# Kernel tuning notes

Measured on AMD Instinct MI355X. Metric: run time of the kernel, lower is better.

Reference implementation:

```python
import jax, jax.numpy as jnp
import numpy as np

D_MODEL = 1024
N_HEADS = 16
D_FF = 4096
D_K = D_MODEL // N_HEADS


def _ln(x, g, b, eps=1e-5):
    mu = jnp.mean(x, axis=-1, keepdims=True)
    var = jnp.mean(jnp.square(x - mu), axis=-1, keepdims=True)
    return (x - mu) * jax.lax.rsqrt(var + eps) * g + b


def setup_inputs() -> dict:
    key = jax.random.key(0)
    ks = jax.random.split(key, 16)
    s = 0.02
    inp = {
        "x": jax.random.normal(ks[0], (2, 2048, D_MODEL), dtype=jnp.float32),
        "Wq": jax.random.normal(ks[1], (D_MODEL, D_MODEL), dtype=jnp.float32) * s,
        "bq": jnp.zeros((D_MODEL,), jnp.float32),
        "Wk": jax.random.normal(ks[2], (D_MODEL, D_MODEL), dtype=jnp.float32) * s,
        "bk": jnp.zeros((D_MODEL,), jnp.float32),
        "Wv": jax.random.normal(ks[3], (D_MODEL, D_MODEL), dtype=jnp.float32) * s,
        "bv": jnp.zeros((D_MODEL,), jnp.float32),
        "Wo": jax.random.normal(ks[4], (D_MODEL, D_MODEL), dtype=jnp.float32) * s,
        "bo": jnp.zeros((D_MODEL,), jnp.float32),
        "W1": jax.random.normal(ks[5], (D_MODEL, D_FF), dtype=jnp.float32) * s,
        "b1": jnp.zeros((D_FF,), jnp.float32),
        "W2": jax.random.normal(ks[6], (D_FF, D_MODEL), dtype=jnp.float32) * s,
        "b2": jnp.zeros((D_MODEL,), jnp.float32),
        "g1": jnp.ones((D_MODEL,), jnp.float32),
        "be1": jnp.zeros((D_MODEL,), jnp.float32),
        "g2": jnp.ones((D_MODEL,), jnp.float32),
        "be2": jnp.zeros((D_MODEL,), jnp.float32),
    }
    return inp


def reference(x, Wq, bq, Wk, bk, Wv, bv, Wo, bo, W1, b1, W2, b2, g1, be1, g2, be2):
    B, L, D = x.shape
    # QKV projections -> [B, H, L, d_k]
    q = (x @ Wq + bq).reshape(B, L, N_HEADS, D_K).transpose(0, 2, 1, 3)
    k = (x @ Wk + bk).reshape(B, L, N_HEADS, D_K).transpose(0, 2, 1, 3)
    v = (x @ Wv + bv).reshape(B, L, N_HEADS, D_K).transpose(0, 2, 1, 3)
    scores = jnp.einsum("bhqd,bhkd->bhqk", q, k) / jnp.sqrt(jnp.float32(D_K))
    attn = jax.nn.softmax(scores, axis=-1)
    ctx = jnp.einsum("bhqk,bhkd->bhqd", attn, v)
    ctx = ctx.transpose(0, 2, 1, 3).reshape(B, L, D)
    attn_out = ctx @ Wo + bo
    # residual + LN1
    h = _ln(x + attn_out, g1, be1)
    # FFN (exact GELU, matching torch F.gelu default)
    ff = jax.nn.gelu(h @ W1 + b1, approximate=False) @ W2 + b2
    return _ln(h + ff, g2, be2)
```

## Files before the change

kernel.cpp:

```cpp
#include <hip/hip_runtime.h>
#include <cmath>


typedef unsigned short u16;
typedef unsigned int u32;
typedef __attribute__((ext_vector_type(8))) __bf16 bf16x8;
typedef __attribute__((ext_vector_type(4))) float f32x4;

#define MFMA16(a, b, c) __builtin_amdgcn_mfma_f32_16x16x32_bf16(a, b, c, 0, 0, 0)

__device__ __forceinline__ u16 f2bf(float f) {
  u32 u = __builtin_bit_cast(u32, f);
  u += 0x7fffu + ((u >> 16) & 1u);
  return (u16)(u >> 16);
}

__device__ __forceinline__ u32 packtrunc(float lo, float hi) {
#if __has_builtin(__builtin_amdgcn_perm)
  return __builtin_amdgcn_perm(__builtin_bit_cast(u32, hi),
                               __builtin_bit_cast(u32, lo), 0x07060302u);
#else
  return (__builtin_bit_cast(u32, lo) >> 16) |
         (__builtin_bit_cast(u32, hi) & 0xFFFF0000u);
#endif
}

__device__ __forceinline__ bf16x8 ld_frag(const u16* p) {
  return __builtin_bit_cast(bf16x8, *(const uint4*)p);
}

__device__ __forceinline__ float fexp2(float x) {
#if __has_builtin(__builtin_amdgcn_exp2f)
  return __builtin_amdgcn_exp2f(x);
#else
  return exp2f(x);
#endif
}

__device__ __forceinline__ void gload16(const u16* g, u16* l) {
  __builtin_amdgcn_global_load_lds(
      (const __attribute__((address_space(1))) void*)g,
      (__attribute__((address_space(3))) void*)l, 16, 0, 0);
}

#define WAITVL(N) asm volatile("s_waitcnt vmcnt(" #N ") lgkmcnt(0)" ::: "memory")
#define BAR() do { __builtin_amdgcn_s_barrier(); asm volatile("" ::: "memory"); } while (0)

__global__ __launch_bounds__(256) void cvt_bf16_k(const float* __restrict__ src,
                                                  u16* __restrict__ dst) {
  int i = (blockIdx.x * 256 + threadIdx.x) * 4;
  float4 v = *(const float4*)(src + i);
  ushort4 o;
  o.x = f2bf(v.x); o.y = f2bf(v.y); o.z = f2bf(v.z); o.w = f2bf(v.w);
  *(ushort4*)(dst + i) = o;
}

__global__ __launch_bounds__(256) void transpose_bf16_k(const float* __restrict__ src,
                                                        u16* __restrict__ dst,
                                                        int R, int C) {
  __shared__ float tile[32][33];
  int tx = threadIdx.x & 31, ty = threadIdx.x >> 5;
  int c0 = blockIdx.x * 32, r0 = blockIdx.y * 32;
#pragma unroll
  for (int i = 0; i < 4; i++)
    tile[ty + 8 * i][tx] = src[(long)(r0 + ty + 8 * i) * C + c0 + tx];
  __syncthreads();
#pragma unroll
  for (int i = 0; i < 4; i++)
    dst[(long)(c0 + ty + 8 * i) * R + r0 + tx] = f2bf(tile[tx][ty + 8 * i]);
}

__global__ __launch_bounds__(256) void transpose4_bf16_k(
    const float* __restrict__ Wq, const float* __restrict__ Wk,
    const float* __restrict__ Wv, const float* __restrict__ Wo,
    u16* __restrict__ wqkvT, u16* __restrict__ woT) {
  const int z = blockIdx.z;
  const float* src = (z == 0) ? Wq : (z == 1) ? Wk : (z == 2) ? Wv : Wo;
  u16* dst = (z < 3) ? (wqkvT + (size_t)z * 1024 * 1024) : woT;
  __shared__ float tile[32][33];
  int tx = threadIdx.x & 31, ty = threadIdx.x >> 5;
  int c0 = blockIdx.x * 32, r0 = blockIdx.y * 32;
#pragma unroll
  for (int i = 0; i < 4; i++)
    tile[ty + 8 * i][tx] = src[(long)(r0 + ty + 8 * i) * 1024 + c0 + tx];
  __syncthreads();
#pragma unroll
  for (int i = 0; i < 4; i++)
    dst[(long)(c0 + ty + 8 * i) * 1024 + r0 + tx] = f2bf(tile[tx][ty + 8 * i]);
}

template <int MODE>
__global__ __launch_bounds__(512, 2) void gemm256_k(
    const u16* __restrict__ A, const u16* __restrict__ BT,
    int N, int lda, int ldb, int Kc,
    const float* __restrict__ bias, float* __restrict__ outF, u16* __restrict__ outB,
    float* __restrict__ p1, float* __restrict__ p2, float* __restrict__ p3,
    u16* __restrict__ qd, u16* __restrict__ kd, u16* __restrict__ vTd,
    const float* __restrict__ bq, const float* __restrict__ bk, const float* __restrict__ bv) {
  __shared__ u16 As[4][256 * 32];
  __shared__ u16 Bs[4][256 * 32];
  const int tid = threadIdx.x;
  const int wave = tid >> 6, lane = tid & 63, quad = lane >> 4, l16 = lane & 15;
  const int wm = wave >> 2, wn = wave & 3;
  const int m0 = blockIdx.y * 256, n0 = blockIdx.x * 256;
  const int kz = blockIdx.z;
  const long kofs = (long)kz * Kc;
  const int KT = Kc >> 5;

  const int srow = lane >> 2;
  const int sseg = (lane & 3) ^ (srow & 3);
  const u16* aS = A + (long)(m0 + wave * 32 + srow) * lda + kofs + sseg * 8;
  const u16* bS = BT + (long)(n0 + wave * 32 + srow) * ldb + kofs + sseg * 8;

  auto stageA = [&](int sb, int s) {
    const u16* p = aS + (long)s * 32;
    gload16(p, &As[sb][wave * 1024]);
    gload16(p + 16 * (long)lda, &As[sb][wave * 1024 + 512]);
  };
  auto stageB = [&](int sb, int s) {
    const u16* p = bS + (long)s * 32;
    gload16(p, &Bs[sb][wave * 1024]);
    gload16(p + 16 * (long)ldb, &Bs[sb][wave * 1024 + 512]);
  };

  int aro[8], bro[4];
#pragma unroll
  for (int mf = 0; mf < 8; mf++) {
    int r = wm * 128 + mf * 16 + l16;
    aro[mf] = r * 32 + ((quad ^ (r & 3)) * 8);
  }
#pragma unroll
  for (int nf = 0; nf < 4; nf++) {
    int r = wn * 64 + nf * 16 + l16;
    bro[nf] = r * 32 + ((quad ^ (r & 3)) * 8);
  }

  f32x4 acc[8][4] = {};

  stageA(0, 0); stageB(0, 0);
  stageA(1, 1); stageB(1, 1);
  stageA(2, 2); stageB(2, 2);

#pragma unroll 1
  for (int t = 0; t < KT; ++t) {
    const int buf = t & 3;
    if (t < KT - 2)      { WAITVL(8); }
    else if (t == KT - 2){ WAITVL(4); }
    else                 { WAITVL(0); }
    BAR();

    bf16x8 af[4], bf4[4];
#pragma unroll
    for (int i = 0; i < 4; i++) af[i] = ld_frag(&As[buf][aro[i]]);
#pragma unroll
    for (int i = 0; i < 4; i++) bf4[i] = ld_frag(&Bs[buf][bro[i]]);
    if (t + 3 < KT) stageA((t + 3) & 3, t + 3);
    BAR();
    __builtin_amdgcn_s_setprio(1);
#pragma unroll
    for (int mf = 0; mf < 4; mf++)
#pragma unroll
      for (int nf = 0; nf < 4; nf++)
        acc[mf][nf] = MFMA16(af[mf], bf4[nf], acc[mf][nf]);
    __builtin_amdgcn_s_setprio(0);

    bf16x8 ag[4];
#pragma unroll
    for (int i = 0; i < 4; i++) ag[i] = ld_frag(&As[buf][aro[4 + i]]);
    if (t + 3 < KT) stageB((t + 3) & 3, t + 3);
    BAR();
    __builtin_amdgcn_s_setprio(1);
#pragma unroll
    for (int mf = 0; mf < 4; mf++)
#pragma unroll
      for (int nf = 0; nf < 4; nf++)
        acc[4 + mf][nf] = MFMA16(ag[mf], bf4[nf], acc[4 + mf][nf]);
    __builtin_amdgcn_s_setprio(0);
  }

  if (MODE == 0) {
    const int nbase = n0 + wn * 64;
    const int mat = nbase >> 10;
    const float* bp = (mat == 0) ? bq : ((mat == 1) ? bk : bv);
    float bb[4];
    int hh0[4], dd0[4];
#pragma unroll
    for (int nf = 0; nf < 4; nf++) {
      int nn = (nbase + nf * 16 + l16) & 1023;
      bb[nf] = bp[nn];
      hh0[nf] = nn >> 6;
      dd0[nf] = nn & 63;
    }
    if (mat < 2) {
#pragma unroll
      for (int mf = 0; mf < 8; mf++) {
#pragma unroll
        for (int r = 0; r < 4; r++) {
          int mr = m0 + wm * 128 + mf * 16 + quad * 4 + r;
          int bI = mr >> 11, ll = mr & 2047;
#pragma unroll
          for (int nf = 0; nf < 4; nf++) {
            float v = acc[mf][nf][r] + bb[nf];
            long idx = ((long)((bI * 16 + hh0[nf]) * 2048 + ll)) * 64 + dd0[nf];
            if (mat == 0) {
              qd[idx] = f2bf(v * 0.18033688011112043f);
            } else {
              kd[idx] = f2bf(v);
            }
          }
        }
      }
    } else {
#pragma unroll
      for (int nf = 0; nf < 4; nf++) {
#pragma unroll
        for (int mf = 0; mf < 8; mf++) {
#pragma unroll
          for (int r = 0; r < 4; r++) {
            int mr = m0 + wm * 128 + mf * 16 + quad * 4 + r;
            int bI = mr >> 11, ll = mr & 2047;
            float v = acc[mf][nf][r] + bb[nf];
            vTd[((long)((bI * 16 + hh0[nf]) * 64 + dd0[nf])) * 2048 + ll] = f2bf(v);
          }
        }
      }
    }
  } else if (MODE == 2) {
    float bb[4];
#pragma unroll
    for (int nf = 0; nf < 4; nf++) bb[nf] = bias[n0 + wn * 64 + nf * 16 + l16];
#pragma unroll
    for (int mf = 0; mf < 8; mf++) {
#pragma unroll
      for (int r = 0; r < 4; r++) {
        int mr = m0 + wm * 128 + mf * 16 + quad * 4 + r;
        u16* orow = outB + (long)mr * N + n0 + wn * 64 + l16;
#pragma unroll
        for (int nf = 0; nf < 4; nf++) {
          float v = acc[mf][nf][r] + bb[nf];
          v = 0.5f * v * (1.0f + erff(v * 0.70710678118654752f));
          orow[nf * 16] = f2bf(v);
        }
      }
    }
  } else {
    float* sl = (kz == 0) ? outF : (kz == 1) ? p1 : (kz == 2) ? p2 : p3;
#pragma unroll
    for (int mf = 0; mf < 8; mf++) {
#pragma unroll
      for (int r = 0; r < 4; r++) {
        int mr = m0 + wm * 128 + mf * 16 + quad * 4 + r;
        float* orow = sl + (long)mr * N + n0 + wn * 64 + l16;
#pragma unroll
        for (int nf = 0; nf < 4; nf++) orow[nf * 16] = acc[mf][nf][r];
      }
    }
  }
}

template <int MODE, int TN>
__global__ __launch_bounds__(256) void gemm_k(
    const u16* __restrict__ A, const u16* __restrict__ BT, int M, int N, int K,
    const float* __restrict__ bias, float* __restrict__ outF, u16* __restrict__ outB,
    u16* __restrict__ qd, u16* __restrict__ kd, u16* __restrict__ vTd,
    const float* __restrict__ bq, const float* __restrict__ bk, const float* __restrict__ bv) {
  constexpr int NT = TN / 32;
  __shared__ u16 As[2][128 * 32];
  __shared__ u16 Bs[2][TN * 32];
  const int tid = threadIdx.x;
  const int wave = tid >> 6, lane = tid & 63, quad = lane >> 4, l16 = lane & 15;
  const int wm = wave >> 1, wn = wave & 1;
  const int m0 = blockIdx.y * 128, n0 = blockIdx.x * TN;

  const int srow = lane >> 2;
  const int sxor = (lane & 3) ^ (srow & 3);
  const u16* aS0 = A + (long)(m0 + wave * 32 + srow) * K + sxor * 8;
  const u16* aS1 = aS0 + 16 * K;
  const u16* bS0 = BT + (long)(n0 + (TN == 128 ? wave * 32 : wave * 16) + srow) * K + sxor * 8;
  const u16* bS1 = bS0 + 16 * K;

  int aoff[4], boff[NT];
#pragma unroll
  for (int t = 0; t < 4; t++) {
    int ra = wm * 64 + t * 16 + l16;
    aoff[t] = ra * 32 + ((quad ^ (l16 & 3)) * 8);
  }
#pragma unroll
  for (int t = 0; t < NT; t++) {
    int rb = wn * (TN / 2) + t * 16 + l16;
    boff[t] = rb * 32 + ((quad ^ (l16 & 3)) * 8);
  }

  auto stage = [&](int buf, int k0) {
    gload16(aS0 + k0, &As[buf][(wave * 2 + 0) * 512]);
    gload16(aS1 + k0, &As[buf][(wave * 2 + 1) * 512]);
    if (TN == 128) {
      gload16(bS0 + k0, &Bs[buf][(wave * 2 + 0) * 512]);
      gload16(bS1 + k0, &Bs[buf][(wave * 2 + 1) * 512]);
    } else {
      gload16(bS0 + k0, &Bs[buf][wave * 512]);
    }
  };

  f32x4 acc[4][NT] = {};

  stage(0, 0);
#pragma unroll 1
  for (int k0 = 0; k0 < K; k0 += 32) {
    const int buf = (k0 >> 5) & 1;
    __syncthreads();
    if (k0 + 32 < K) stage(buf ^ 1, k0 + 32);
    bf16x8 af[4], bfr[NT];
#pragma unroll
    for (int t = 0; t < 4; t++) af[t] = ld_frag(&As[buf][aoff[t]]);
#pragma unroll
    for (int t = 0; t < NT; t++) bfr[t] = ld_frag(&Bs[buf][boff[t]]);
#pragma unroll
    for (int mt = 0; mt < 4; mt++)
#pragma unroll
      for (int nt = 0; nt < NT; nt++)
        acc[mt][nt] = MFMA16(af[mt], bfr[nt], acc[mt][nt]);
  }

  if (MODE == 1) {
    float bb[NT];
#pragma unroll
    for (int nt = 0; nt < NT; nt++) bb[nt] = bias[n0 + wn * (TN / 2) + nt * 16 + l16];
#pragma unroll
    for (int mt = 0; mt < 4; mt++) {
#pragma unroll
      for (int r = 0; r < 4; r++) {
        int mr = m0 + wm * 64 + mt * 16 + quad * 4 + r;
        float* orow = outF + (long)mr * N + n0 + wn * (TN / 2) + l16;
#pragma unroll
        for (int nt = 0; nt < NT; nt++)
          orow[nt * 16] = acc[mt][nt][r] + bb[nt];
      }
    }
  }
}

__global__ __launch_bounds__(256) void attn_k(const u16* __restrict__ qd,
                                              const u16* __restrict__ kd,
                                              const u16* __restrict__ vTd,
                                              float* __restrict__ oP0,
                                              float* __restrict__ oP1,
                                              float* __restrict__ ml0,
                                              float* __restrict__ ml1) {
  __shared__ u16 Ks[2][64 * 64];
  __shared__ u16 Vs[2][64 * 64];
  __shared__ __align__(16) u16 P[4][32][72];
  const int tid = threadIdx.x;
  const int wave = tid >> 6, lane = tid & 63, quad = lane >> 4, l16 = lane & 15;
  const int bh = blockIdx.y;
  const int kz = blockIdx.z;
  const int jbeg = kz * 1024, jend = jbeg + 1024;
  const u16* Q = qd + (long)bh * 2048 * 64;
  const u16* Kp = kd + (long)bh * 2048 * 64;
  const u16* Vt = vTd + (long)bh * 64 * 2048;
  const int qbase = blockIdx.x * 128 + wave * 32;

  bf16x8 qf[2][2];
#pragma unroll
  for (int qs = 0; qs < 2; qs++) {
    qf[qs][0] = ld_frag(Q + (qbase + qs * 16 + l16) * 64 + quad * 8);
    qf[qs][1] = ld_frag(Q + (qbase + qs * 16 + l16) * 64 + 32 + quad * 8);
  }

  f32x4 o[2][4] = {};
  float m[2] = {-1e30f, -1e30f}, l[2] = {0.f, 0.f};

  const int srow = lane >> 3;
  const int sx = (lane & 7) ^ srow;
  const int kr0 = wave * 16 + srow;
  const int kr1 = wave * 16 + 8 + srow;

  const int fs0 = ((0 * 4 + quad) ^ (l16 & 7)) * 8;
  const int fs1 = ((1 * 4 + quad) ^ (l16 & 7)) * 8;

  auto stage = [&](int buf, int j0) {
    gload16(Kp + (long)(j0 + kr0) * 64 + sx * 8, &Ks[buf][(wave * 2 + 0) * 512]);
    gload16(Kp + (long)(j0 + kr1) * 64 + sx * 8, &Ks[buf][(wave * 2 + 1) * 512]);
    gload16(Vt + (long)kr0 * 2048 + j0 + sx * 8, &Vs[buf][(wave * 2 + 0) * 512]);
    gload16(Vt + (long)kr1 * 2048 + j0 + sx * 8, &Vs[buf][(wave * 2 + 1) * 512]);
  };

  stage(0, jbeg);

#pragma unroll 1
  for (int j0 = jbeg; j0 < jend; j0 += 64) {
    const int buf = (j0 >> 6) & 1;
    __syncthreads();
    if (j0 + 64 < jend) stage(buf ^ 1, j0 + 64);

    const u16* kb = &Ks[buf][0];
    f32x4 st[2][4];
#pragma unroll
    for (int f = 0; f < 4; f++) {
      bf16x8 k0 = ld_frag(kb + (f * 16 + l16) * 64 + fs0);
      bf16x8 k1 = ld_frag(kb + (f * 16 + l16) * 64 + fs1);
      f32x4 s0 = {}, s1 = {};
      s0 = MFMA16(k0, qf[0][0], s0); s0 = MFMA16(k1, qf[0][1], s0);
      s1 = MFMA16(k0, qf[1][0], s1); s1 = MFMA16(k1, qf[1][1], s1);
      st[0][f] = s0; st[1][f] = s1;
    }

#pragma unroll
    for (int qs = 0; qs < 2; qs++) {
      float mx = -1e30f;
#pragma unroll
      for (int f = 0; f < 4; f++)
        mx = fmaxf(mx, fmaxf(fmaxf(st[qs][f][0], st[qs][f][1]),
                             fmaxf(st[qs][f][2], st[qs][f][3])));
      mx = fmaxf(mx, __shfl_xor(mx, 16));
      mx = fmaxf(mx, __shfl_xor(mx, 32));
      if (__any(mx > m[qs] + 8.0f)) {
        float mn = fmaxf(m[qs], mx);
        float al = fexp2(m[qs] - mn);
        m[qs] = mn;
        l[qs] *= al;
#pragma unroll
        for (int nt = 0; nt < 4; nt++) {
          o[qs][nt][0] *= al; o[qs][nt][1] *= al;
          o[qs][nt][2] *= al; o[qs][nt][3] *= al;
        }
      }
      float sm = 0.f;
      u16* prow = &P[wave][qs * 16 + l16][0];
#pragma unroll
      for (int f = 0; f < 4; f++) {
        float p0 = fexp2(st[qs][f][0] - m[qs]);
        float p1 = fexp2(st[qs][f][1] - m[qs]);
        float p2 = fexp2(st[qs][f][2] - m[qs]);
        float p3 = fexp2(st[qs][f][3] - m[qs]);
        sm += (p0 + p1) + (p2 + p3);
        uint2 u;
        u.x = packtrunc(p0, p1);
        u.y = packtrunc(p2, p3);
        *(uint2*)(prow + f * 16 + quad * 4) = u;
      }
      sm += __shfl_xor(sm, 16);
      sm += __shfl_xor(sm, 32);
      l[qs] += sm;
    }
    __asm__ volatile("s_waitcnt lgkmcnt(0)" ::: "memory");

    const u16* vb = &Vs[buf][0];
    bf16x8 vf[4][2];
#pragma unroll
    for (int nt = 0; nt < 4; nt++) {
      vf[nt][0] = ld_frag(vb + (nt * 16 + l16) * 64 + fs0);
      vf[nt][1] = ld_frag(vb + (nt * 16 + l16) * 64 + fs1);
    }
#pragma unroll
    for (int qs = 0; qs < 2; qs++) {
      const u16* prow = &P[wave][qs * 16 + l16][0];
#pragma unroll
      for (int kh = 0; kh < 2; kh++) {
        bf16x8 pf = ld_frag(prow + kh * 32 + quad * 8);
#pragma unroll
        for (int nt = 0; nt < 4; nt++)
          o[qs][nt] = MFMA16(vf[nt][kh], pf, o[qs][nt]);
      }
    }
  }

  float* oDst = kz ? oP1 : oP0;
  float* mlDst = kz ? ml1 : ml0;
#pragma unroll
  for (int qs = 0; qs < 2; qs++) {
    const long row = (long)bh * 2048 + qbase + qs * 16 + l16;
#pragma unroll
    for (int nt = 0; nt < 4; nt++)
      *(float4*)(oDst + row * 64 + nt * 16 + quad * 4) =
          *(const float4*)&o[qs][nt];
    if (quad == 0) {
      float2 ml2 = {m[qs], l[qs]};
      *(float2*)(mlDst + row * 2) = ml2;
    }
  }
}

__global__ __launch_bounds__(256) void attn_combine_k(
    const float* __restrict__ o0, const float* __restrict__ o1,
    const float* __restrict__ ml0, const float* __restrict__ ml1,
    u16* __restrict__ ctx) {
  long i = ((long)blockIdx.x * 256 + threadIdx.x) * 4;
  long row = i >> 6;
  int d = (int)(i & 63);
  float2 a0 = *(const float2*)(ml0 + row * 2);
  float2 a1 = *(const float2*)(ml1 + row * 2);
  float M = fmaxf(a0.x, a1.x);
  float w0 = fexp2(a0.x - M), w1 = fexp2(a1.x - M);
  float rinv = 1.0f / (a0.y * w0 + a1.y * w1);
  float4 v0 = *(const float4*)(o0 + i);
  float4 v1 = *(const float4*)(o1 + i);
  int bh = (int)(row >> 11), ll = (int)(row & 2047);
  int bI = bh >> 4, hh = bh & 15;
  ushort4 w;
  w.x = f2bf((v0.x * w0 + v1.x * w1) * rinv);
  w.y = f2bf((v0.y * w0 + v1.y * w1) * rinv);
  w.z = f2bf((v0.z * w0 + v1.z * w1) * rinv);
  w.w = f2bf((v0.w * w0 + v1.w * w1) * rinv);
  *(ushort4*)(ctx + ((long)(bI * 2048 + ll) * 1024) + hh * 64 + d) = w;
}

__global__ __launch_bounds__(256) void ln_k(const float* __restrict__ a,
                                            const float* __restrict__ b,
                                            const float* __restrict__ g,
                                            const float* __restrict__ be,
                                            float* __restrict__ outF,
                                            u16* __restrict__ outB) {
  const int row = blockIdx.x, tid = threadIdx.x;
  const float* pa = a + (long)row * 1024;
  const float* pb = b + (long)row * 1024;
  float v[4], s = 0.f, sq = 0.f;
#pragma unroll
  for (int i = 0; i < 4; i++) {
    int c = i * 256 + tid;
    v[i] = pa[c] + pb[c];
    s += v[i];
    sq += v[i] * v[i];
  }
#pragma unroll
  for (int off = 1; off < 64; off <<= 1) {
    s += __shfl_xor(s, off);
    sq += __shfl_xor(sq, off);
  }
  __shared__ float red[10];
  int wave = tid >> 6, lane = tid & 63;
  if (lane == 0) { red[wave * 2] = s; red[wave * 2 + 1] = sq; }
  __syncthreads();
  if (tid == 0) {
    float S = red[0] + red[2] + red[4] + red[6];
    float Q = red[1] + red[3] + red[5] + red[7];
    float mu = S * (1.0f / 1024.0f);
    float var = Q * (1.0f / 1024.0f) - mu * mu;
    red[8] = mu;
    red[9] = rsqrtf(var + 1e-5f);
  }
  __syncthreads();
  float mu = red[8], rstd = red[9];
#pragma unroll
  for (int i = 0; i < 4; i++) {
    int c = i * 256 + tid;
    float o = (v[i] - mu) * rstd * g[c] + be[c];
    outF[(long)row * 1024 + c] = o;
    if (outB) outB[(long)row * 1024 + c] = f2bf(o);
  }
}

__global__ __launch_bounds__(256) void ln4_k(const float* __restrict__ a,
                                             const float* __restrict__ q0,
                                             const float* __restrict__ q1,
                                             const float* __restrict__ q2,
                                             const float* __restrict__ q3,
                                             const float* __restrict__ bias,
                                             const float* __restrict__ g,
                                             const float* __restrict__ be,
                                             float* __restrict__ outF) {
  const int row = blockIdx.x, tid = threadIdx.x;
  const long base = (long)row * 1024;
  float v[4], s = 0.f, sq = 0.f;
#pragma unroll
  for (int i = 0; i < 4; i++) {
    int c = i * 256 + tid;
    float ff = (q0[base + c] + q1[base + c]) + (q2[base + c] + q3[base + c]) + bias[c];
    v[i] = a[base + c] + ff;
    s += v[i];
    sq += v[i] * v[i];
  }
#pragma unroll
  for (int off = 1; off < 64; off <<= 1) {
    s += __shfl_xor(s, off);
    sq += __shfl_xor(sq, off);
  }
  __shared__ float red[10];
  int wave = tid >> 6, lane = tid & 63;
  if (lane == 0) { red[wave * 2] = s; red[wave * 2 + 1] = sq; }
  __syncthreads();
  if (tid == 0) {
    float S = red[0] + red[2] + red[4] + red[6];
    float Q = red[1] + red[3] + red[5] + red[7];
    float mu = S * (1.0f / 1024.0f);
    float var = Q * (1.0f / 1024.0f) - mu * mu;
    red[8] = mu;
    red[9] = rsqrtf(var + 1e-5f);
  }
  __syncthreads();
  float mu = red[8], rstd = red[9];
#pragma unroll
  for (int i = 0; i < 4; i++) {
    int c = i * 256 + tid;
    outF[base + c] = (v[i] - mu) * rstd * g[c] + be[c];
  }
}

extern "C" void kernel_launch(void* const* d_in, const int* in_sizes, int n_in,
                              void* d_out, int out_size, void* d_ws, size_t ws_size,
                              hipStream_t stream) {
  const float* x  = (const float*)d_in[0];
  const float* Wq = (const float*)d_in[1];  const float* bq = (const float*)d_in[2];
  const float* Wk = (const float*)d_in[3];  const float* bk = (const float*)d_in[4];
  const float* Wv = (const float*)d_in[5];  const float* bv = (const float*)d_in[6];
  const float* Wo = (const float*)d_in[7];  const float* bo = (const float*)d_in[8];
  const float* W1 = (const float*)d_in[9];  const float* b1 = (const float*)d_in[10];
  const float* W2 = (const float*)d_in[11]; const float* b2 = (const float*)d_in[12];
  const float* g1 = (const float*)d_in[13]; const float* be1 = (const float*)d_in[14];
  const float* g2 = (const float*)d_in[15]; const float* be2 = (const float*)d_in[16];

  char* ws = (char*)d_ws;
  size_t off = 0;
  auto alloc = [&](size_t bytes) {
    size_t o = off;
    off += (bytes + 255) & ~(size_t)255;
    return o;
  };
  u16*   xb     = (u16*)(ws + alloc(4096UL * 1024 * 2));
  u16*   wqkvT  = (u16*)(ws + alloc(3072UL * 1024 * 2));
  u16*   woT    = (u16*)(ws + alloc(1024UL * 1024 * 2));
  u16*   w1T    = (u16*)(ws + alloc(4096UL * 1024 * 2));
  u16*   w2T    = (u16*)(ws + alloc(1024UL * 4096 * 2));
  u16*   qb     = (u16*)(ws + alloc(32UL * 2048 * 64 * 2));
  u16*   kb     = (u16*)(ws + alloc(32UL * 2048 * 64 * 2));
  u16*   vTb    = (u16*)(ws + alloc(32UL * 64 * 2048 * 2));
  u16*   ctx    = (u16*)(ws + alloc(4096UL * 1024 * 2));
  float* attnO  = (float*)(ws + alloc(4096UL * 1024 * 4));
  float* h      = (float*)(ws + alloc(4096UL * 1024 * 4));
  u16*   hb     = (u16*)(ws + alloc(4096UL * 1024 * 2));
  u16*   ff1    = (u16*)(ws + alloc(4096UL * 4096 * 2));
  float* ff2    = (float*)(ws + alloc(4096UL * 1024 * 4));
  if (off > ws_size) return;

  float* oPart0 = attnO;
  float* oPart1 = h;
  float* mlP0   = (float*)hb;
  float* mlP1   = (float*)hb + 32 * 2048 * 2;

  float* sl0 = ff2;
  float* sl1 = attnO;
  float* sl2 = (float*)qb;
  float* sl3 = (float*)vTb;

  cvt_bf16_k<<<4096, 256, 0, stream>>>(x, xb);
  transpose4_bf16_k<<<dim3(32, 32, 4), 256, 0, stream>>>(Wq, Wk, Wv, Wo, wqkvT, woT);
  transpose_bf16_k<<<dim3(128, 32), 256, 0, stream>>>(W1, w1T, 1024, 4096);
  transpose_bf16_k<<<dim3(32, 128), 256, 0, stream>>>(W2, w2T, 4096, 1024);

  gemm256_k<0><<<dim3(12, 16), 512, 0, stream>>>(
      xb, wqkvT, 3072, 1024, 1024, 1024,
      nullptr, nullptr, nullptr, nullptr, nullptr, nullptr,
      qb, kb, vTb, bq, bk, bv);
  attn_k<<<dim3(16, 32, 2), 256, 0, stream>>>(qb, kb, vTb,
                                              oPart0, oPart1, mlP0, mlP1);
  attn_combine_k<<<4096, 256, 0, stream>>>(oPart0, oPart1, mlP0, mlP1, ctx);
  gemm_k<1, 64><<<dim3(16, 32), 256, 0, stream>>>(ctx, woT, 4096, 1024, 1024,
                                                  bo, attnO, nullptr,
                                                  nullptr, nullptr, nullptr, nullptr, nullptr, nullptr);
  ln_k<<<4096, 256, 0, stream>>>(x, attnO, g1, be1, h, hb);
  gemm256_k<2><<<dim3(16, 16), 512, 0, stream>>>(
      hb, w1T, 4096, 1024, 1024, 1024,
      b1, nullptr, ff1, nullptr, nullptr, nullptr,
      nullptr, nullptr, nullptr, nullptr, nullptr, nullptr);
  gemm256_k<3><<<dim3(4, 16, 4), 512, 0, stream>>>(
      ff1, w2T, 1024, 4096, 4096, 1024,
      nullptr, sl0, nullptr, sl1, sl2, sl3,
      nullptr, nullptr, nullptr, nullptr, nullptr, nullptr);
  ln4_k<<<4096, 256, 0, stream>>>(h, sl0, sl1, sl2, sl3, b2, g2, be2, (float*)d_out);
}
```

Measured before the change: 399.0 us.

## Keep attention P in registers via lane shuffles; split-K Wo GEMM with fused LN

The attention kernel no longer writes the softmax probabilities to shared memory and reads them back. Packed bf16 values are exchanged between lanes with shuffles to form the PV MFMA operand, and the V fragment swizzle is adjusted to match the permuted k ordering. The output-projection GEMM now reuses the 256-tile split-K kernel with four partial slices, and a unified LN kernel sums the partials plus bias. This removes LDS traffic and a wait in attention and gives the Wo GEMM more blocks, in exchange for extra partial-sum memory traffic in the LN step.

```diff
diff --git a/kernel.cpp b/kernel.cpp
--- a/kernel.cpp
+++ b/kernel.cpp
@@ -258,98 +258,15 @@
   }
 }
 
-template <int MODE, int TN>
-__global__ __launch_bounds__(256) void gemm_k(
-    const u16* __restrict__ A, const u16* __restrict__ BT, int M, int N, int K,
-    const float* __restrict__ bias, float* __restrict__ outF, u16* __restrict__ outB,
-    u16* __restrict__ qd, u16* __restrict__ kd, u16* __restrict__ vTd,
-    const float* __restrict__ bq, const float* __restrict__ bk, const float* __restrict__ bv) {
-  constexpr int NT = TN / 32;
-  __shared__ u16 As[2][128 * 32];
-  __shared__ u16 Bs[2][TN * 32];
-  const int tid = threadIdx.x;
-  const int wave = tid >> 6, lane = tid & 63, quad = lane >> 4, l16 = lane & 15;
-  const int wm = wave >> 1, wn = wave & 1;
-  const int m0 = blockIdx.y * 128, n0 = blockIdx.x * TN;
-
-  const int srow = lane >> 2;
-  const int sxor = (lane & 3) ^ (srow & 3);
-  const u16* aS0 = A + (long)(m0 + wave * 32 + srow) * K + sxor * 8;
-  const u16* aS1 = aS0 + 16 * K;
-  const u16* bS0 = BT + (long)(n0 + (TN == 128 ? wave * 32 : wave * 16) + srow) * K + sxor * 8;
-  const u16* bS1 = bS0 + 16 * K;
-
-  int aoff[4], boff[NT];
-#pragma unroll
-  for (int t = 0; t < 4; t++) {
-    int ra = wm * 64 + t * 16 + l16;
-    aoff[t] = ra * 32 + ((quad ^ (l16 & 3)) * 8);
-  }
-#pragma unroll
-  for (int t = 0; t < NT; t++) {
-    int rb = wn * (TN / 2) + t * 16 + l16;
-    boff[t] = rb * 32 + ((quad ^ (l16 & 3)) * 8);
-  }
-
-  auto stage = [&](int buf, int k0) {
-    gload16(aS0 + k0, &As[buf][(wave * 2 + 0) * 512]);
-    gload16(aS1 + k0, &As[buf][(wave * 2 + 1) * 512]);
-    if (TN == 128) {
-      gload16(bS0 + k0, &Bs[buf][(wave * 2 + 0) * 512]);
-      gload16(bS1 + k0, &Bs[buf][(wave * 2 + 1) * 512]);
-    } else {
-      gload16(bS0 + k0, &Bs[buf][wave * 512]);
-    }
-  };
-
-  f32x4 acc[4][NT] = {};
-
-  stage(0, 0);
-#pragma unroll 1
-  for (int k0 = 0; k0 < K; k0 += 32) {
-    const int buf = (k0 >> 5) & 1;
-    __syncthreads();
-    if (k0 + 32 < K) stage(buf ^ 1, k0 + 32);
-    bf16x8 af[4], bfr[NT];
-#pragma unroll
-    for (int t = 0; t < 4; t++) af[t] = ld_frag(&As[buf][aoff[t]]);
-#pragma unroll
-    for (int t = 0; t < NT; t++) bfr[t] = ld_frag(&Bs[buf][boff[t]]);
-#pragma unroll
-    for (int mt = 0; mt < 4; mt++)
-#pragma unroll
-      for (int nt = 0; nt < NT; nt++)
-        acc[mt][nt] = MFMA16(af[mt], bfr[nt], acc[mt][nt]);
-  }
-
-  if (MODE == 1) {
-    float bb[NT];
-#pragma unroll
-    for (int nt = 0; nt < NT; nt++) bb[nt] = bias[n0 + wn * (TN / 2) + nt * 16 + l16];
-#pragma unroll
-    for (int mt = 0; mt < 4; mt++) {
-#pragma unroll
-      for (int r = 0; r < 4; r++) {
-        int mr = m0 + wm * 64 + mt * 16 + quad * 4 + r;
-        float* orow = outF + (long)mr * N + n0 + wn * (TN / 2) + l16;
-#pragma unroll
-        for (int nt = 0; nt < NT; nt++)
-          orow[nt * 16] = acc[mt][nt][r] + bb[nt];
-      }
-    }
-  }
-}
-
-__global__ __launch_bounds__(256) void attn_k(const u16* __restrict__ qd,
-                                              const u16* __restrict__ kd,
-                                              const u16* __restrict__ vTd,
-                                              float* __restrict__ oP0,
-                                              float* __restrict__ oP1,
-                                              float* __restrict__ ml0,
-                                              float* __restrict__ ml1) {
+__global__ __launch_bounds__(256, 4) void attn_k(const u16* __restrict__ qd,
+                                                 const u16* __restrict__ kd,
+                                                 const u16* __restrict__ vTd,
+                                                 float* __restrict__ oP0,
+                                                 float* __restrict__ oP1,
+                                                 float* __restrict__ ml0,
+                                                 float* __restrict__ ml1) {
   __shared__ u16 Ks[2][64 * 64];
   __shared__ u16 Vs[2][64 * 64];
-  __shared__ __align__(16) u16 P[4][32][72];
   const int tid = threadIdx.x;
   const int wave = tid >> 6, lane = tid & 63, quad = lane >> 4, l16 = lane & 15;
   const int bh = blockIdx.y;
@@ -377,6 +294,9 @@
 
   const int fs0 = ((0 * 4 + quad) ^ (l16 & 7)) * 8;
   const int fs1 = ((1 * 4 + quad) ^ (l16 & 7)) * 8;
+  const int sV = ((quad & 1) << 1) | (quad >> 1);
+  const int fv0 = ((0 * 4 + sV) ^ (l16 & 7)) * 8;
+  const int fv1 = ((1 * 4 + sV) ^ (l16 & 7)) * 8;
 
   auto stage = [&](int buf, int j0) {
     gload16(Kp + (long)(j0 + kr0) * 64 + sx * 8, &Ks[buf][(wave * 2 + 0) * 512]);
@@ -403,6 +323,14 @@
       s0 = MFMA16(k0, qf[0][0], s0); s0 = MFMA16(k1, qf[0][1], s0);
       s1 = MFMA16(k0, qf[1][0], s1); s1 = MFMA16(k1, qf[1][1], s1);
       st[0][f] = s0; st[1][f] = s1;
+    }
+
+    const u16* vb = &Vs[buf][0];
+    bf16x8 vf[4][2];
+#pragma unroll
+    for (int nt = 0; nt < 4; nt++) {
+      vf[nt][0] = ld_frag(vb + (nt * 16 + l16) * 64 + fv0);
+      vf[nt][1] = ld_frag(vb + (nt * 16 + l16) * 64 + fv1);
     }
 
 #pragma unroll
@@ -426,7 +354,7 @@
         }
       }
       float sm = 0.f;
-      u16* prow = &P[wave][qs * 16 + l16][0];
+      u32 wp[4][2];
 #pragma unroll
       for (int f = 0; f < 4; f++) {
         float p0 = fexp2(st[qs][f][0] - m[qs]);
@@ -434,30 +362,26 @@
         float p2 = fexp2(st[qs][f][2] - m[qs]);
         float p3 = fexp2(st[qs][f][3] - m[qs]);
         sm += (p0 + p1) + (p2 + p3);
-        uint2 u;
-        u.x = packtrunc(p0, p1);
-        u.y = packtrunc(p2, p3);
-        *(uint2*)(prow + f * 16 + quad * 4) = u;
+        wp[f][0] = packtrunc(p0, p1);
+        wp[f][1] = packtrunc(p2, p3);
       }
       sm += __shfl_xor(sm, 16);
       sm += __shfl_xor(sm, 32);
       l[qs] += sm;
-    }
-    __asm__ volatile("s_waitcnt lgkmcnt(0)" ::: "memory");
-
-    const u16* vb = &Vs[buf][0];
-    bf16x8 vf[4][2];
-#pragma unroll
-    for (int nt = 0; nt < 4; nt++) {
-      vf[nt][0] = ld_frag(vb + (nt * 16 + l16) * 64 + fs0);
-      vf[nt][1] = ld_frag(vb + (nt * 16 + l16) * 64 + fs1);
-    }
-#pragma unroll
-    for (int qs = 0; qs < 2; qs++) {
-      const u16* prow = &P[wave][qs * 16 + l16][0];
+
 #pragma unroll
       for (int kh = 0; kh < 2; kh++) {
-        bf16x8 pf = ld_frag(prow + kh * 32 + quad * 8);
+        const int flo = kh * 2, fhi = flo + 1;
+        u32 tx0 = (quad & 1) ? wp[flo][0] : wp[fhi][0];
+        u32 tx1 = (quad & 1) ? wp[flo][1] : wp[fhi][1];
+        u32 rx0 = __shfl_xor(tx0, 16);
+        u32 rx1 = __shfl_xor(tx1, 16);
+        uint4 fw;
+        fw.x = (quad & 1) ? rx0 : wp[flo][0];
+        fw.y = (quad & 1) ? rx1 : wp[flo][1];
+        fw.z = (quad & 1) ? wp[fhi][0] : rx0;
+        fw.w = (quad & 1) ? wp[fhi][1] : rx1;
+        bf16x8 pf = __builtin_bit_cast(bf16x8, fw);
 #pragma unroll
         for (int nt = 0; nt < 4; nt++)
           o[qs][nt] = MFMA16(vf[nt][kh], pf, o[qs][nt]);
@@ -505,20 +429,24 @@
   *(ushort4*)(ctx + ((long)(bI * 2048 + ll) * 1024) + hh * 64 + d) = w;
 }
 
-__global__ __launch_bounds__(256) void ln_k(const float* __restrict__ a,
-                                            const float* __restrict__ b,
-                                            const float* __restrict__ g,
-                                            const float* __restrict__ be,
-                                            float* __restrict__ outF,
-                                            u16* __restrict__ outB) {
+__global__ __launch_bounds__(256) void ln4b_k(const float* __restrict__ a,
+                                              const float* __restrict__ q0,
+                                              const float* __restrict__ q1,
+                                              const float* __restrict__ q2,
+                                              const float* __restrict__ q3,
+                                              const float* __restrict__ bias,
+                                              const float* __restrict__ g,
+                                              const float* __restrict__ be,
+                                              float* __restrict__ outF,
+                                              u16* __restrict__ outB) {
   const int row = blockIdx.x, tid = threadIdx.x;
-  const float* pa = a + (long)row * 1024;
-  const float* pb = b + (long)row * 1024;
+  const long base = (long)row * 1024;
   float v[4], s = 0.f, sq = 0.f;
 #pragma unroll
   for (int i = 0; i < 4; i++) {
     int c = i * 256 + tid;
-    v[i] = pa[c] + pb[c];
+    float ff = (q0[base + c] + q1[base + c]) + (q2[base + c] + q3[base + c]) + bias[c];
+    v[i] = a[base + c] + ff;
     s += v[i];
     sq += v[i] * v[i];
   }
@@ -545,54 +473,8 @@
   for (int i = 0; i < 4; i++) {
     int c = i * 256 + tid;
     float o = (v[i] - mu) * rstd * g[c] + be[c];
-    outF[(long)row * 1024 + c] = o;
-    if (outB) outB[(long)row * 1024 + c] = f2bf(o);
-  }
-}
-
-__global__ __launch_bounds__(256) void ln4_k(const float* __restrict__ a,
-                                             const float* __restrict__ q0,
-                                             const float* __restrict__ q1,
-                                             const float* __restrict__ q2,
-                                             const float* __restrict__ q3,
-                                             const float* __restrict__ bias,
-                                             const float* __restrict__ g,
-                                             const float* __restrict__ be,
-                                             float* __restrict__ outF) {
-  const int row = blockIdx.x, tid = threadIdx.x;
-  const long base = (long)row * 1024;
-  float v[4], s = 0.f, sq = 0.f;
-#pragma unroll
-  for (int i = 0; i < 4; i++) {
-    int c = i * 256 + tid;
-    float ff = (q0[base + c] + q1[base + c]) + (q2[base + c] + q3[base + c]) + bias[c];
-    v[i] = a[base + c] + ff;
-    s += v[i];
-    sq += v[i] * v[i];
-  }
-#pragma unroll
-  for (int off = 1; off < 64; off <<= 1) {
-    s += __shfl_xor(s, off);
-    sq += __shfl_xor(sq, off);
-  }
-  __shared__ float red[10];
-  int wave = tid >> 6, lane = tid & 63;
-  if (lane == 0) { red[wave * 2] = s; red[wave * 2 + 1] = sq; }
-  __syncthreads();
-  if (tid == 0) {
-    float S = red[0] + red[2] + red[4] + red[6];
-    float Q = red[1] + red[3] + red[5] + red[7];
-    float mu = S * (1.0f / 1024.0f);
-    float var = Q * (1.0f / 1024.0f) - mu * mu;
-    red[8] = mu;
-    red[9] = rsqrtf(var + 1e-5f);
-  }
-  __syncthreads();
-  float mu = red[8], rstd = red[9];
-#pragma unroll
-  for (int i = 0; i < 4; i++) {
-    int c = i * 256 + tid;
-    outF[base + c] = (v[i] - mu) * rstd * g[c] + be[c];
+    outF[base + c] = o;
+    if (outB) outB[base + c] = f2bf(o);
   }
 }
 
@@ -637,6 +519,11 @@
   float* mlP0   = (float*)hb;
   float* mlP1   = (float*)hb + 32 * 2048 * 2;
 
+  float* wl0 = attnO;
+  float* wl1 = ff2;
+  float* wl2 = (float*)ff1;
+  float* wl3 = (float*)ff1 + 4UL * 1024 * 1024;
+
   float* sl0 = ff2;
   float* sl1 = attnO;
   float* sl2 = (float*)qb;
@@ -654,10 +541,11 @@
   attn_k<<<dim3(16, 32, 2), 256, 0, stream>>>(qb, kb, vTb,
                                               oPart0, oPart1, mlP0, mlP1);
   attn_combine_k<<<4096, 256, 0, stream>>>(oPart0, oPart1, mlP0, mlP1, ctx);
-  gemm_k<1, 64><<<dim3(16, 32), 256, 0, stream>>>(ctx, woT, 4096, 1024, 1024,
-                                                  bo, attnO, nullptr,
-                                                  nullptr, nullptr, nullptr, nullptr, nullptr, nullptr);
-  ln_k<<<4096, 256, 0, stream>>>(x, attnO, g1, be1, h, hb);
+  gemm256_k<3><<<dim3(4, 16, 4), 512, 0, stream>>>(
+      ctx, woT, 1024, 1024, 1024, 256,
+      nullptr, wl0, nullptr, wl1, wl2, wl3,
+      nullptr, nullptr, nullptr, nullptr, nullptr, nullptr);
+  ln4b_k<<<4096, 256, 0, stream>>>(x, wl0, wl1, wl2, wl3, bo, g1, be1, h, hb);
   gemm256_k<2><<<dim3(16, 16), 512, 0, stream>>>(
       hb, w1T, 4096, 1024, 1024, 1024,
       b1, nullptr, ff1, nullptr, nullptr, nullptr,
@@ -666,5 +554,6 @@
       ff1, w2T, 1024, 4096, 4096, 1024,
       nullptr, sl0, nullptr, sl1, sl2, sl3,
       nullptr, nullptr, nullptr, nullptr, nullptr, nullptr);
-  ln4_k<<<4096, 256, 0, stream>>>(h, sl0, sl1, sl2, sl3, b2, g2, be2, (float*)d_out);
-}
+  ln4b_k<<<4096, 256, 0, stream>>>(h, sl0, sl1, sl2, sl3, b2, g2, be2,
+                                   (float*)d_out, nullptr);
+}
```

Measured after the change: 420.1 us. +5.3%, slower.
